# Kernel optimization log

Hardware: AMD Instinct MI355X
Metric: run time of the kernel (lower is better)

Reference implementation:

```python
import jax, jax.numpy as jnp
import numpy as np

N_ENTITIES = 100000
N_EDGES = 500000
N_RELATIONS = 200
DIM = 64
HEADS = 4
POW_ITER = 5
ALPHA = 0.1
LEAKY_SLOPE = 0.01
EPS = 1e-16


def setup_inputs() -> dict:
    key = jax.random.key(0)
    ks = jax.random.split(key, 11)
    scale = 0.1
    return {
        "entity_embed": jax.random.normal(ks[0], (N_ENTITIES, DIM), jnp.float32),
        "relation_embed": jax.random.normal(ks[1], (N_RELATIONS, DIM), jnp.float32),
        "W_h": jax.random.normal(ks[2], (DIM, HEADS * DIM), jnp.float32) * scale,
        "W_t": jax.random.normal(ks[3], (DIM, HEADS * DIM), jnp.float32) * scale,
        "W_r": jax.random.normal(ks[4], (DIM, HEADS * DIM), jnp.float32) * scale,
        "att_h": jax.random.normal(ks[5], (HEADS, DIM), jnp.float32) * scale,
        "att_t": jax.random.normal(ks[6], (HEADS, DIM), jnp.float32) * scale,
        "att_r": jax.random.normal(ks[7], (HEADS, DIM), jnp.float32) * scale,
        "W_o": jax.random.normal(ks[8], (HEADS * DIM, DIM), jnp.float32) * scale,
        "edge_index": jax.random.randint(ks[9], (2, N_EDGES), 0, N_ENTITIES, jnp.int64),
        "edge_type": jax.random.randint(ks[10], (N_EDGES,), 0, N_RELATIONS, jnp.int64),
    }


def _segment_softmax(scores, seg_ids, num_segments):
    # scores: [E, heads]; softmax over edges sharing the same seg_id, per head
    m = jax.ops.segment_max(scores, seg_ids, num_segments=num_segments)
    e = jnp.exp(scores - m[seg_ids])
    denom = jax.ops.segment_sum(e, seg_ids, num_segments=num_segments)
    return e / (denom[seg_ids] + EPS)


def reference(entity_embed, relation_embed, W_h, W_t, W_r,
              att_h, att_t, att_r, W_o, edge_index, edge_type):
    head_ids, tail_ids = edge_index[0], edge_index[1]

    # per-edge gathered embeddings, projected per head: [E, heads, dim]
    Wh = (entity_embed[head_ids] @ W_h).reshape(-1, HEADS, DIM)
    Wt = (entity_embed[tail_ids] @ W_t).reshape(-1, HEADS, DIM)
    Wr = (relation_embed[edge_type] @ W_r).reshape(-1, HEADS, DIM)

    s_h = jnp.sum(jnp.tanh(Wh) * att_h[None], axis=-1)  # [E, heads]
    s_t = jnp.sum(jnp.tanh(Wt) * att_t[None], axis=-1)
    s_r = jnp.sum(jnp.tanh(Wr) * att_r[None], axis=-1)
    scores = jax.nn.leaky_relu(s_h + s_t + s_r, negative_slope=LEAKY_SLOPE)

    att = _segment_softmax(scores, head_ids, N_ENTITIES)  # [E, heads]
    A = (1.0 - ALPHA) * att

    # PPR power iteration, vectorized over heads: Z: [N, heads, dim]
    Z0 = entity_embed[:, None, :]  # [N, 1, dim]
    Z_init = jnp.broadcast_to(Z0, (N_ENTITIES, HEADS, DIM))

    def step(Z, _):
        msgs = A[:, :, None] * Z[tail_ids]  # [E, heads, dim]
        Z_new = jax.ops.segment_sum(msgs, head_ids, num_segments=N_ENTITIES) + ALPHA * Z0
        return Z_new, None

    Z, _ = jax.lax.scan(step, Z_init, None, length=POW_ITER)

    out = Z.reshape(N_ENTITIES, HEADS * DIM) @ W_o  # [N, dim]
    return out
```

## Files before the change

### kernel.cpp

```cpp
#include <hip/hip_runtime.h>
#include <hip/hip_fp16.h>
#include <math.h>

#define N_ENT 100000
#define N_EDGE 500000
#define N_REL 200

typedef short bf16x8 __attribute__((ext_vector_type(8)));
typedef _Float16 f16x8 __attribute__((ext_vector_type(8)));
typedef float f32x4 __attribute__((ext_vector_type(4)));

__device__ __forceinline__ float fast_tanh(float x) {
    float xc = fminf(x, 15.f);
    float e = __expf(2.f * xc);
    return 1.f - 2.f * __builtin_amdgcn_rcpf(e + 1.f);
}

__device__ __forceinline__ unsigned short f2bf(float f) {
    unsigned u = __float_as_uint(f);
    unsigned r = u + 0x7FFF + ((u >> 16) & 1);
    return (unsigned short)(r >> 16);
}

__device__ __forceinline__ unsigned pack_half2(float a, float b) {
    __half2 h = __floats2half2_rn(a, b);
    return *reinterpret_cast<unsigned*>(&h);
}

#define HIST_B 1954
#define EMB_B  2048
#define WT_B   128
#define WOT_B  64
__global__ __launch_bounds__(256) void prep_kernel(
    const float* __restrict__ entity, unsigned short* __restrict__ emb_bf,
    const float* __restrict__ W0, const float* __restrict__ W1,
    unsigned short* __restrict__ wT,
    const float* __restrict__ Wo, __half* __restrict__ woT,
    const int* __restrict__ eidx, int* __restrict__ counts,
    int* __restrict__ eoff)
{
    int bid = blockIdx.x;
    if (bid < HIST_B) {
        int e = bid * 256 + threadIdx.x;
        if (e < N_EDGE) eoff[e] = atomicAdd(&counts[eidx[e]], 1);
    } else if (bid < HIST_B + EMB_B) {
        int b = bid - HIST_B;
        const int nquads = N_ENT * 64 / 4;
        for (int i = b * 256 + threadIdx.x; i < nquads; i += EMB_B * 256) {
            float4 v = ((const float4*)entity)[i];
            ushort4 o;
            o.x = f2bf(v.x); o.y = f2bf(v.y); o.z = f2bf(v.z); o.w = f2bf(v.w);
            ((ushort4*)emb_bf)[i] = o;
        }
    } else if (bid < HIST_B + EMB_B + WT_B) {
        int idx = (bid - HIST_B - EMB_B) * 256 + threadIdx.x;
        int mat = idx >> 14;
        int rem = idx & 16383;
        int col = rem >> 6;
        int k   = rem & 63;
        const float* W = (mat == 0) ? W0 : W1;
        wT[idx] = f2bf(W[k * 256 + col]);
    } else {
        int idx = (bid - HIST_B - EMB_B - WT_B) * 256 + threadIdx.x;
        int d = idx >> 8;
        int k = idx & 255;
        woT[idx] = __float2half(Wo[k * 64 + d]);
    }
}

__global__ __launch_bounds__(256) void proj_mfma_kernel(
    const unsigned short* __restrict__ emb_bf,
    const unsigned short* __restrict__ wT,
    const float* __restrict__ att0, const float* __restrict__ att1,
    float* __restrict__ p0, float* __restrict__ p1, int nrows, int nb)
{
    const int mat = (blockIdx.x >= nb) ? 1 : 0;
    const int rb  = blockIdx.x - mat * nb;
    const float* att = (mat == 0) ? att0 : att1;
    float* p         = (mat == 0) ? p0 : p1;
    const unsigned short* wbase = wT + (size_t)mat * 256 * 64;

    const int wv   = threadIdx.x >> 6;
    const int lane = threadIdx.x & 63;
    const int r4   = lane >> 4;
    const int cl   = lane & 15;
    const int rowbase = rb * 64 + wv * 16;

    int ra = min(rowbase + cl, nrows - 1);
    bf16x8 a0 = *(const bf16x8*)(emb_bf + (size_t)ra * 64 + 8 * r4);
    bf16x8 a1 = *(const bf16x8*)(emb_bf + (size_t)ra * 64 + 8 * r4 + 32);

    float pacc[4][4];
#pragma unroll
    for (int head = 0; head < 4; ++head) {
        float vsum[4] = {0.f, 0.f, 0.f, 0.f};
#pragma unroll
        for (int sub = 0; sub < 4; ++sub) {
            int col = head * 64 + sub * 16 + cl;
            const unsigned short* wp = wbase + (size_t)col * 64 + 8 * r4;
            bf16x8 b0 = *(const bf16x8*)(wp);
            bf16x8 b1 = *(const bf16x8*)(wp + 32);
            f32x4 c = {0.f, 0.f, 0.f, 0.f};
            c = __builtin_amdgcn_mfma_f32_16x16x32_bf16(a0, b0, c, 0, 0, 0);
            c = __builtin_amdgcn_mfma_f32_16x16x32_bf16(a1, b1, c, 0, 0, 0);
            float av = att[head * 64 + sub * 16 + cl];
#pragma unroll
            for (int j = 0; j < 4; ++j)
                vsum[j] = fmaf(fast_tanh(c[j]), av, vsum[j]);
        }
#pragma unroll
        for (int j = 0; j < 4; ++j) {
            float v = vsum[j];
            v += __shfl_xor(v, 1, 64);
            v += __shfl_xor(v, 2, 64);
            v += __shfl_xor(v, 4, 64);
            v += __shfl_xor(v, 8, 64);
            pacc[head][j] = v;
        }
    }
    if (cl == 0) {
#pragma unroll
        for (int j = 0; j < 4; ++j) {
            int row = rowbase + r4 * 4 + j;
            if (row < nrows) {
                *(float4*)(p + (size_t)row * 4) = make_float4(
                    pacc[0][j], pacc[1][j], pacc[2][j], pacc[3][j]);
            }
        }
    }
}

__global__ __launch_bounds__(256) void proj_gemm_kernel(
    const float* __restrict__ emb,
    const float* __restrict__ W0,
    const float* __restrict__ att0,
    float* __restrict__ p0,
    int nrows)
{
    __shared__ float e_lds[64][68];
    __shared__ float w0_lds[64][64];
    __shared__ float red[4][4][64];

    const int t    = threadIdx.x;
    const int wv   = t >> 6;
    const int lane = t & 63;
    const int er   = t & 15;
    const int d0   = (t >> 4) * 4;
    const int base = blockIdx.x * 64;

#pragma unroll
    for (int i = 0; i < 4; ++i) {
        int f = t + 256 * i;
        int row = f >> 4, c4 = f & 15;
        int gr = min(base + row, nrows - 1);
        float4 v = *(const float4*)(emb + (size_t)gr * 64 + 4 * c4);
        *(float4*)&e_lds[row][4 * c4] = v;
    }

    float p0s[4][4];

    for (int head = 0; head < 4; ++head) {
        {
            int k0 = t >> 4, c4 = t & 15;
#pragma unroll
            for (int kk = 0; kk < 4; ++kk) {
                int k = k0 + 16 * kk;
                *(float4*)&w0_lds[k][4 * c4] =
                    *(const float4*)(W0 + (size_t)k * 256 + head * 64 + 4 * c4);
            }
        }
        __syncthreads();

        float acc0[4][4] = {};
        for (int k4 = 0; k4 < 16; ++k4) {
            float4 z0 = *(const float4*)&e_lds[er +  0][4 * k4];
            float4 z1 = *(const float4*)&e_lds[er + 16][4 * k4];
            float4 z2 = *(const float4*)&e_lds[er + 32][4 * k4];
            float4 z3 = *(const float4*)&e_lds[er + 48][4 * k4];
            const float zr[4][4] = {
                {z0.x, z0.y, z0.z, z0.w},
                {z1.x, z1.y, z1.z, z1.w},
                {z2.x, z2.y, z2.z, z2.w},
                {z3.x, z3.y, z3.z, z3.w}};
#pragma unroll
            for (int jj = 0; jj < 4; ++jj) {
                float4 w0v = *(const float4*)&w0_lds[4 * k4 + jj][d0];
#pragma unroll
                for (int i = 0; i < 4; ++i) {
                    float zj = zr[i][jj];
                    acc0[i][0] = fmaf(zj, w0v.x, acc0[i][0]);
                    acc0[i][1] = fmaf(zj, w0v.y, acc0[i][1]);
                    acc0[i][2] = fmaf(zj, w0v.z, acc0[i][2]);
                    acc0[i][3] = fmaf(zj, w0v.w, acc0[i][3]);
                }
            }
        }

        float4 av0 = *(const float4*)(att0 + head * 64 + d0);
#pragma unroll
        for (int i = 0; i < 4; ++i) {
            float v = fast_tanh(acc0[i][0]) * av0.x
                    + fast_tanh(acc0[i][1]) * av0.y
                    + fast_tanh(acc0[i][2]) * av0.z
                    + fast_tanh(acc0[i][3]) * av0.w;
            v += __shfl_xor(v, 16, 64);
            v += __shfl_xor(v, 32, 64);
            p0s[head][i] = v;
        }
        __syncthreads();
    }

    if (lane < 16) {
#pragma unroll
        for (int h = 0; h < 4; ++h)
#pragma unroll
            for (int i = 0; i < 4; ++i)
                red[wv][h][lane + 16 * i] = p0s[h][i];
    }
    __syncthreads();
    if (t < 64) {
        int row = base + t;
        if (row < nrows) {
            float4 pv;
            pv.x = red[0][0][t] + red[1][0][t] + red[2][0][t] + red[3][0][t];
            pv.y = red[0][1][t] + red[1][1][t] + red[2][1][t] + red[3][1][t];
            pv.z = red[0][2][t] + red[1][2][t] + red[2][2][t] + red[3][2][t];
            pv.w = red[0][3][t] + red[1][3][t] + red[2][3][t] + red[3][3][t];
            *(float4*)(p0 + (size_t)row * 4) = pv;
        }
    }
}

__global__ __launch_bounds__(1024) void scan_kernel(
    const int* __restrict__ counts, int* __restrict__ row_start)
{
    __shared__ int wsum[16];
    __shared__ int carry_s;
    const int lane = threadIdx.x & 63;
    const int wid  = threadIdx.x >> 6;
    if (threadIdx.x == 0) carry_s = 0;
    __syncthreads();
    for (int base = 0; base < N_ENT; base += 4096) {
        int i0 = base + (int)threadIdx.x * 4;
        int4 v = make_int4(0, 0, 0, 0);
        if (i0 + 3 < N_ENT) v = *(const int4*)(counts + i0);
        else {
            if (i0 + 0 < N_ENT) v.x = counts[i0 + 0];
            if (i0 + 1 < N_ENT) v.y = counts[i0 + 1];
            if (i0 + 2 < N_ENT) v.z = counts[i0 + 2];
            if (i0 + 3 < N_ENT) v.w = counts[i0 + 3];
        }
        int s1 = v.x + v.y, s2 = s1 + v.z, tsum = s2 + v.w;
        int incl = tsum;
#pragma unroll
        for (int off = 1; off < 64; off <<= 1) {
            int t = __shfl_up(incl, off, 64);
            if (lane >= off) incl += t;
        }
        if (lane == 63) wsum[wid] = incl;
        __syncthreads();
        int wave_off = 0;
#pragma unroll
        for (int w = 0; w < 16; ++w)
            wave_off += (w < wid) ? wsum[w] : 0;
        int carry = carry_s;
        int excl = carry + wave_off + (incl - tsum);
        if (i0 + 3 < N_ENT) {
            *(int4*)(row_start + i0) = make_int4(excl, excl + v.x, excl + s1, excl + s2);
        } else {
            if (i0 + 0 < N_ENT) row_start[i0 + 0] = excl;
            if (i0 + 1 < N_ENT) row_start[i0 + 1] = excl + v.x;
            if (i0 + 2 < N_ENT) row_start[i0 + 2] = excl + s1;
            if (i0 + 3 < N_ENT) row_start[i0 + 3] = excl + s2;
        }
        __syncthreads();
        if (threadIdx.x == 1023) carry_s = carry + wave_off + incl;
    }
    __syncthreads();
    if (threadIdx.x == 0) row_start[N_ENT] = carry_s;
}

__global__ __launch_bounds__(256) void scatter_score_kernel(
    const int* __restrict__ eidx, const int* __restrict__ etype,
    const float* __restrict__ ph, const float* __restrict__ pt,
    const float* __restrict__ pr,
    const int* __restrict__ row_start, const int* __restrict__ eoff,
    int* __restrict__ csr_col, float* __restrict__ csr_a)
{
    int e = blockIdx.x * 256 + threadIdx.x;
    if (e >= N_EDGE) return;
    int hn = eidx[e];
    int tn = eidx[N_EDGE + e];
    int r  = etype[e];
    float4 a = *(const float4*)(ph + (size_t)hn * 4);
    float4 b = *(const float4*)(pt + (size_t)tn * 4);
    float4 c = *(const float4*)(pr + (size_t)r * 4);
    float s0 = a.x + b.x + c.x;
    float s1 = a.y + b.y + c.y;
    float s2 = a.z + b.z + c.z;
    float s3 = a.w + b.w + c.w;
    s0 = s0 >= 0.f ? s0 : 0.01f * s0;
    s1 = s1 >= 0.f ? s1 : 0.01f * s1;
    s2 = s2 >= 0.f ? s2 : 0.01f * s2;
    s3 = s3 >= 0.f ? s3 : 0.01f * s3;
    float4 ev = make_float4(__expf(s0), __expf(s1), __expf(s2), __expf(s3));
    int pos = row_start[hn] + eoff[e];
    csr_col[pos] = tn;
    *(float4*)(csr_a + (size_t)pos * 4) = ev;
}

template <bool IN_HALF, bool NORM>
__device__ __forceinline__ void spmm_row_pair(
    int n, int lane, float scale,
    const __half* __restrict__ Zin_h, const float* __restrict__ emb,
    const int* __restrict__ row_start, const int* __restrict__ csr_col,
    float* __restrict__ csr_a, float acc[8])
{
    const int half = lane >> 5;
    const int j    = lane & 31;
    const int hd   = j >> 3;
    const int s    = row_start[n];
    const int end  = row_start[n + 1];

    {
        const float* z0p = emb + (size_t)n * 64 + 8 * (j & 7);
        float4 z0a = *(const float4*)(z0p);
        float4 z0b = *(const float4*)(z0p + 4);
        float m = (half == 0) ? 0.1f : 0.f;
        acc[0] = m * z0a.x; acc[1] = m * z0a.y; acc[2] = m * z0a.z; acc[3] = m * z0a.w;
        acc[4] = m * z0b.x; acc[5] = m * z0b.y; acc[6] = m * z0b.z; acc[7] = m * z0b.w;
    }
    float accB[8] = {0.f, 0.f, 0.f, 0.f, 0.f, 0.f, 0.f, 0.f};

    for (int b = s; b < end; b += 16) {
        const int nb = min(16, end - b);
        int   cl = (lane < nb) ? csr_col[b + lane] : 0;
        float al = (lane < nb * 4) ? csr_a[(size_t)b * 4 + lane] : 0.f;
        if (NORM) {
            al *= scale;
            if (lane < nb * 4) csr_a[(size_t)b * 4 + lane] = al;
        }
        for (int e = 0; e < nb; e += 4) {
            int iA = half ? min(e + 1, nb - 1) : e;
            int iB = half ? min(e + 3, nb - 1) : min(e + 2, nb - 1);
            int cA = __shfl(cl, iA, 64);
            int cB = __shfl(cl, iB, 64);
            float aA = __shfl(al, iA * 4 + hd, 64);
            float aB = __shfl(al, iB * 4 + hd, 64);
            aA = (e + half < nb) ? aA : 0.f;
            aB = (e + 2 + half < nb) ? aB : 0.f;
            if (IN_HALF) {
                f16x8 zA = *(const f16x8*)(Zin_h + (size_t)cA * 256 + 8 * j);
                f16x8 zB = *(const f16x8*)(Zin_h + (size_t)cB * 256 + 8 * j);
#pragma unroll
                for (int k = 0; k < 8; ++k) {
                    acc[k]  = fmaf(aA, (float)zA[k], acc[k]);
                    accB[k] = fmaf(aB, (float)zB[k], accB[k]);
                }
            } else {
                int ec = 8 * (j & 7);
                float4 zA0 = *(const float4*)(emb + (size_t)cA * 64 + ec);
                float4 zA1 = *(const float4*)(emb + (size_t)cA * 64 + ec + 4);
                float4 zB0 = *(const float4*)(emb + (size_t)cB * 64 + ec);
                float4 zB1 = *(const float4*)(emb + (size_t)cB * 64 + ec + 4);
                acc[0] = fmaf(aA, zA0.x, acc[0]);
                acc[1] = fmaf(aA, zA0.y, acc[1]);
                acc[2] = fmaf(aA, zA0.z, acc[2]);
                acc[3] = fmaf(aA, zA0.w, acc[3]);
                acc[4] = fmaf(aA, zA1.x, acc[4]);
                acc[5] = fmaf(aA, zA1.y, acc[5]);
                acc[6] = fmaf(aA, zA1.z, acc[6]);
                acc[7] = fmaf(aA, zA1.w, acc[7]);
                accB[0] = fmaf(aB, zB0.x, accB[0]);
                accB[1] = fmaf(aB, zB0.y, accB[1]);
                accB[2] = fmaf(aB, zB0.z, accB[2]);
                accB[3] = fmaf(aB, zB0.w, accB[3]);
                accB[4] = fmaf(aB, zB1.x, accB[4]);
                accB[5] = fmaf(aB, zB1.y, accB[5]);
                accB[6] = fmaf(aB, zB1.z, accB[6]);
                accB[7] = fmaf(aB, zB1.w, accB[7]);
            }
        }
    }
#pragma unroll
    for (int k = 0; k < 8; ++k) {
        float v = acc[k] + accB[k];
        v += __shfl_xor(v, 32, 64);
        acc[k] = v;
    }
}

__device__ __forceinline__ void store_row_h(
    __half* __restrict__ dst256, int lane, const float acc[8])
{
    if (lane < 32) {
        uint4 o;
        o.x = pack_half2(acc[0], acc[1]);
        o.y = pack_half2(acc[2], acc[3]);
        o.z = pack_half2(acc[4], acc[5]);
        o.w = pack_half2(acc[6], acc[7]);
        *(uint4*)(dst256 + 8 * lane) = o;
    }
}

__global__ __launch_bounds__(256) void norm_spmm1_kernel(
    const float* __restrict__ emb,
    const int* __restrict__ row_start, const int* __restrict__ csr_col,
    float* __restrict__ csr_a, __half* __restrict__ Zout)
{
    const int wave = threadIdx.x >> 6;
    const int lane = threadIdx.x & 63;
    const int n = blockIdx.x * 4 + wave;
    const int s   = row_start[n];
    const int end = row_start[n + 1];
    const int nf  = (end - s) * 4;

    float sum = 0.f;
    for (int f = lane; f < nf; f += 64)
        sum += csr_a[(size_t)s * 4 + f];
#pragma unroll
    for (int off = 4; off < 64; off <<= 1)
        sum += __shfl_xor(sum, off, 64);
    float scale = 0.9f * __builtin_amdgcn_rcpf(sum + 1e-16f);

    float acc[8];
    spmm_row_pair<false, true>(n, lane, scale, nullptr, emb,
                               row_start, csr_col, csr_a, acc);
    store_row_h(Zout + (size_t)n * 256, lane, acc);
}

__global__ __launch_bounds__(256) void spmm_kernel(
    const __half* __restrict__ Zin, const float* __restrict__ emb,
    const int* __restrict__ row_start, const int* __restrict__ csr_col,
    float* __restrict__ csr_a, __half* __restrict__ Zout)
{
    const int wave = threadIdx.x >> 6;
    const int lane = threadIdx.x & 63;
    const int n = blockIdx.x * 4 + wave;
    float acc[8];
    spmm_row_pair<true, false>(n, lane, 1.f, Zin, emb,
                               row_start, csr_col, csr_a, acc);
    store_row_h(Zout + (size_t)n * 256, lane, acc);
}

__global__ __launch_bounds__(256) void spmm_out_fused_kernel(
    const __half* __restrict__ Zin, const float* __restrict__ emb,
    const int* __restrict__ row_start, const int* __restrict__ csr_col,
    float* __restrict__ csr_a,
    const __half* __restrict__ woT,
    float* __restrict__ out)
{
    __shared__ _Float16 zl[16][264];
    const int wv   = threadIdx.x >> 6;
    const int lane = threadIdx.x & 63;
    const int base = blockIdx.x * 16;

#pragma unroll
    for (int rr = 0; rr < 4; ++rr) {
        int n = base + wv * 4 + rr;
        float acc[8];
        spmm_row_pair<true, false>(n, lane, 1.f, Zin, emb,
                                   row_start, csr_col, csr_a, acc);
        if (lane < 32) {
            uint4 o;
            o.x = pack_half2(acc[0], acc[1]);
            o.y = pack_half2(acc[2], acc[3]);
            o.z = pack_half2(acc[4], acc[5]);
            o.w = pack_half2(acc[6], acc[7]);
            *(uint4*)&zl[wv * 4 + rr][8 * lane] = o;
        }
    }
    __syncthreads();

    const int cl = lane & 15;
    const int r4 = lane >> 4;
    f16x8 a[8];
#pragma unroll
    for (int ks = 0; ks < 8; ++ks)
        a[ks] = *(const f16x8*)&zl[cl][ks * 32 + 8 * r4];

    const _Float16* wcol = (const _Float16*)woT + (size_t)(wv * 16 + cl) * 256 + 8 * r4;
    f32x4 c = {0.f, 0.f, 0.f, 0.f};
#pragma unroll
    for (int ks = 0; ks < 8; ++ks) {
        f16x8 b = *(const f16x8*)(wcol + ks * 32);
        c = __builtin_amdgcn_mfma_f32_16x16x32_f16(a[ks], b, c, 0, 0, 0);
    }
#pragma unroll
    for (int j = 0; j < 4; ++j) {
        int row = base + r4 * 4 + j;
        out[(size_t)row * 64 + wv * 16 + cl] = c[j];
    }
}

extern "C" void kernel_launch(void* const* d_in, const int* in_sizes, int n_in,
                              void* d_out, int out_size, void* d_ws, size_t ws_size,
                              hipStream_t stream)
{
    const float* entity = (const float*)d_in[0];
    const float* rel    = (const float*)d_in[1];
    const float* W_h    = (const float*)d_in[2];
    const float* W_t    = (const float*)d_in[3];
    const float* W_r    = (const float*)d_in[4];
    const float* att_h  = (const float*)d_in[5];
    const float* att_t  = (const float*)d_in[6];
    const float* att_r  = (const float*)d_in[7];
    const float* W_o    = (const float*)d_in[8];
    const int*   eidx   = (const int*)d_in[9];
    const int*   etype  = (const int*)d_in[10];
    float* out = (float*)d_out;

    char* ws = (char*)d_ws;
    size_t off = 0;
    auto alloc = [&](size_t bytes) -> void* {
        void* p = ws + off;
        off += (bytes + 255) & ~(size_t)255;
        return p;
    };
    float* p_h      = (float*)alloc((size_t)N_ENT * 4 * 4);
    float* p_t      = (float*)alloc((size_t)N_ENT * 4 * 4);
    float* p_r      = (float*)alloc((size_t)N_REL * 4 * 4);
    int*   counts   = (int*)alloc((size_t)N_ENT * 4);
    int*   row_start= (int*)alloc(((size_t)N_ENT + 1) * 4);
    int*   eoff     = (int*)alloc((size_t)N_EDGE * 4);
    int*   csr_col  = (int*)alloc((size_t)N_EDGE * 4);
    float* csr_a    = (float*)alloc((size_t)N_EDGE * 4 * 4);
    __half* Zh_a    = (__half*)alloc((size_t)N_ENT * 256 * 2);
    __half* Zh_b    = (__half*)alloc((size_t)N_ENT * 256 * 2);
    unsigned short* emb_bf = (unsigned short*)alloc((size_t)N_ENT * 64 * 2);
    unsigned short* wT     = (unsigned short*)alloc((size_t)2 * 256 * 64 * 2);
    __half* woT     = (__half*)alloc((size_t)64 * 256 * 2);

    hipMemsetAsync(counts, 0, (size_t)N_ENT * 4, stream);

    prep_kernel<<<HIST_B + EMB_B + WT_B + WOT_B, 256, 0, stream>>>(
        entity, emb_bf, W_h, W_t, wT, W_o, woT, eidx, counts, eoff);

    const int nb = (N_ENT + 63) / 64;
    proj_mfma_kernel<<<2 * nb, 256, 0, stream>>>(
        emb_bf, wT, att_h, att_t, p_h, p_t, N_ENT, nb);
    proj_gemm_kernel<<<(N_REL + 63) / 64, 256, 0, stream>>>(
        rel, W_r, att_r, p_r, N_REL);

    scan_kernel<<<1, 1024, 0, stream>>>(counts, row_start);
    scatter_score_kernel<<<(N_EDGE + 255) / 256, 256, 0, stream>>>(
        eidx, etype, p_h, p_t, p_r, row_start, eoff, csr_col, csr_a);

    norm_spmm1_kernel<<<N_ENT / 4, 256, 0, stream>>>(
        entity, row_start, csr_col, csr_a, Zh_b);
    spmm_kernel<<<N_ENT / 4, 256, 0, stream>>>(Zh_b, entity, row_start, csr_col, csr_a, Zh_a);
    spmm_kernel<<<N_ENT / 4, 256, 0, stream>>>(Zh_a, entity, row_start, csr_col, csr_a, Zh_b);
    spmm_kernel<<<N_ENT / 4, 256, 0, stream>>>(Zh_b, entity, row_start, csr_col, csr_a, Zh_a);
    spmm_out_fused_kernel<<<N_ENT / 16, 256, 0, stream>>>(
        Zh_a, entity, row_start, csr_col, csr_a, woT, out);
}
```

Baseline: 405.0 us.

## Split SpMM power iterations per head with row-per-8-lanes mapping and fp16 embeddings

Restructures the PPR sparse propagation. A separate normalize kernel rescales the attention weights. Each power iteration now runs as four per-head launches, so the gathered working set for a launch is one 64-wide head slice, which should fit better in L2/infinity cache. Each wave handles 8 rows with 8 lanes per row and walks edges serially. The entity embeddings are also precomputed in fp16, which shrinks the first-iteration gathers and the Z0 reads. This adds 12 extra launches and gives up the per-wave edge-parallel batching, so long rows become serial. The Z0 term loses some precision from the fp16 embeddings.

```diff
diff --git a/kernel.cpp b/kernel.cpp
--- a/kernel.cpp
+++ b/kernel.cpp
@@ -33,6 +33,7 @@
 #define WOT_B  64
 __global__ __launch_bounds__(256) void prep_kernel(
     const float* __restrict__ entity, unsigned short* __restrict__ emb_bf,
+    __half* __restrict__ emb_h,
     const float* __restrict__ W0, const float* __restrict__ W1,
     unsigned short* __restrict__ wT,
     const float* __restrict__ Wo, __half* __restrict__ woT,
@@ -51,6 +52,10 @@
             ushort4 o;
             o.x = f2bf(v.x); o.y = f2bf(v.y); o.z = f2bf(v.z); o.w = f2bf(v.w);
             ((ushort4*)emb_bf)[i] = o;
+            uint2 oh;
+            oh.x = pack_half2(v.x, v.y);
+            oh.y = pack_half2(v.z, v.w);
+            ((uint2*)emb_h)[i] = oh;
         }
     } else if (bid < HIST_B + EMB_B + WT_B) {
         int idx = (bid - HIST_B - EMB_B) * 256 + threadIdx.x;
@@ -309,166 +314,106 @@
     *(float4*)(csr_a + (size_t)pos * 4) = ev;
 }
 
-template <bool IN_HALF, bool NORM>
-__device__ __forceinline__ void spmm_row_pair(
-    int n, int lane, float scale,
-    const __half* __restrict__ Zin_h, const float* __restrict__ emb,
+__global__ __launch_bounds__(256) void normalize_kernel(
+    const int* __restrict__ row_start, float* __restrict__ csr_a)
+{
+    const int wid  = threadIdx.x >> 6;
+    const int lane = threadIdx.x & 63;
+    const int n = blockIdx.x * 4 + wid;
+    if (n >= N_ENT) return;
+    const int s   = row_start[n];
+    const int end = row_start[n + 1];
+    const int nf  = (end - s) * 4;
+
+    float sum = 0.f;
+    for (int f = lane; f < nf; f += 64)
+        sum += csr_a[(size_t)s * 4 + f];
+#pragma unroll
+    for (int off = 4; off < 64; off <<= 1)
+        sum += __shfl_xor(sum, off, 64);
+    float scale = 0.9f * __builtin_amdgcn_rcpf(sum + 1e-16f);
+    for (int f = lane; f < nf; f += 64)
+        csr_a[(size_t)s * 4 + f] *= scale;
+}
+
+template <bool FIRST>
+__global__ __launch_bounds__(256) void spmm_head_kernel(
+    const __half* __restrict__ Zin,
+    const __half* __restrict__ emb_h,
     const int* __restrict__ row_start, const int* __restrict__ csr_col,
-    float* __restrict__ csr_a, float acc[8])
-{
-    const int half = lane >> 5;
-    const int j    = lane & 31;
-    const int hd   = j >> 3;
-    const int s    = row_start[n];
-    const int end  = row_start[n + 1];
-
+    const float* __restrict__ csr_a, __half* __restrict__ Zout, int phase)
+{
+    const int wave = threadIdx.x >> 6;
+    const int lane = threadIdx.x & 63;
+    const int r = lane >> 3;
+    const int c = lane & 7;
+    const int n = (blockIdx.x * 4 + wave) * 8 + r;
+    if (n >= N_ENT) return;
+
+    const _Float16* zin = (const _Float16*)Zin;
+    float acc[8];
     {
-        const float* z0p = emb + (size_t)n * 64 + 8 * (j & 7);
-        float4 z0a = *(const float4*)(z0p);
-        float4 z0b = *(const float4*)(z0p + 4);
-        float m = (half == 0) ? 0.1f : 0.f;
-        acc[0] = m * z0a.x; acc[1] = m * z0a.y; acc[2] = m * z0a.z; acc[3] = m * z0a.w;
-        acc[4] = m * z0b.x; acc[5] = m * z0b.y; acc[6] = m * z0b.z; acc[7] = m * z0b.w;
-    }
-    float accB[8] = {0.f, 0.f, 0.f, 0.f, 0.f, 0.f, 0.f, 0.f};
-
-    for (int b = s; b < end; b += 16) {
-        const int nb = min(16, end - b);
-        int   cl = (lane < nb) ? csr_col[b + lane] : 0;
-        float al = (lane < nb * 4) ? csr_a[(size_t)b * 4 + lane] : 0.f;
-        if (NORM) {
-            al *= scale;
-            if (lane < nb * 4) csr_a[(size_t)b * 4 + lane] = al;
-        }
-        for (int e = 0; e < nb; e += 4) {
-            int iA = half ? min(e + 1, nb - 1) : e;
-            int iB = half ? min(e + 3, nb - 1) : min(e + 2, nb - 1);
-            int cA = __shfl(cl, iA, 64);
-            int cB = __shfl(cl, iB, 64);
-            float aA = __shfl(al, iA * 4 + hd, 64);
-            float aB = __shfl(al, iB * 4 + hd, 64);
-            aA = (e + half < nb) ? aA : 0.f;
-            aB = (e + 2 + half < nb) ? aB : 0.f;
-            if (IN_HALF) {
-                f16x8 zA = *(const f16x8*)(Zin_h + (size_t)cA * 256 + 8 * j);
-                f16x8 zB = *(const f16x8*)(Zin_h + (size_t)cB * 256 + 8 * j);
-#pragma unroll
-                for (int k = 0; k < 8; ++k) {
-                    acc[k]  = fmaf(aA, (float)zA[k], acc[k]);
-                    accB[k] = fmaf(aB, (float)zB[k], accB[k]);
-                }
-            } else {
-                int ec = 8 * (j & 7);
-                float4 zA0 = *(const float4*)(emb + (size_t)cA * 64 + ec);
-                float4 zA1 = *(const float4*)(emb + (size_t)cA * 64 + ec + 4);
-                float4 zB0 = *(const float4*)(emb + (size_t)cB * 64 + ec);
-                float4 zB1 = *(const float4*)(emb + (size_t)cB * 64 + ec + 4);
-                acc[0] = fmaf(aA, zA0.x, acc[0]);
-                acc[1] = fmaf(aA, zA0.y, acc[1]);
-                acc[2] = fmaf(aA, zA0.z, acc[2]);
-                acc[3] = fmaf(aA, zA0.w, acc[3]);
-                acc[4] = fmaf(aA, zA1.x, acc[4]);
-                acc[5] = fmaf(aA, zA1.y, acc[5]);
-                acc[6] = fmaf(aA, zA1.z, acc[6]);
-                acc[7] = fmaf(aA, zA1.w, acc[7]);
-                accB[0] = fmaf(aB, zB0.x, accB[0]);
-                accB[1] = fmaf(aB, zB0.y, accB[1]);
-                accB[2] = fmaf(aB, zB0.z, accB[2]);
-                accB[3] = fmaf(aB, zB0.w, accB[3]);
-                accB[4] = fmaf(aB, zB1.x, accB[4]);
-                accB[5] = fmaf(aB, zB1.y, accB[5]);
-                accB[6] = fmaf(aB, zB1.z, accB[6]);
-                accB[7] = fmaf(aB, zB1.w, accB[7]);
-            }
-        }
-    }
-#pragma unroll
-    for (int k = 0; k < 8; ++k) {
-        float v = acc[k] + accB[k];
-        v += __shfl_xor(v, 32, 64);
-        acc[k] = v;
-    }
-}
-
-__device__ __forceinline__ void store_row_h(
-    __half* __restrict__ dst256, int lane, const float acc[8])
-{
-    if (lane < 32) {
+        f16x8 z0 = *(const f16x8*)((const _Float16*)emb_h + (size_t)n * 64 + 8 * c);
+#pragma unroll
+        for (int k = 0; k < 8; ++k) acc[k] = 0.1f * (float)z0[k];
+    }
+    const int s = row_start[n], end = row_start[n + 1];
+    for (int e = s; e < end; ++e) {
+        float a  = csr_a[(size_t)e * 4 + phase];
+        int col  = csr_col[e];
+        const _Float16* zp = FIRST
+            ? zin + (size_t)col * 64 + 8 * c
+            : zin + (size_t)col * 256 + phase * 64 + 8 * c;
+        f16x8 z = *(const f16x8*)zp;
+#pragma unroll
+        for (int k = 0; k < 8; ++k) acc[k] = fmaf(a, (float)z[k], acc[k]);
+    }
+    uint4 o;
+    o.x = pack_half2(acc[0], acc[1]);
+    o.y = pack_half2(acc[2], acc[3]);
+    o.z = pack_half2(acc[4], acc[5]);
+    o.w = pack_half2(acc[6], acc[7]);
+    *(uint4*)((_Float16*)Zout + (size_t)n * 256 + phase * 64 + 8 * c) = o;
+}
+
+__global__ __launch_bounds__(256) void spmm_out_fused_kernel(
+    const __half* __restrict__ Zin, const __half* __restrict__ emb_h,
+    const int* __restrict__ row_start, const int* __restrict__ csr_col,
+    const float* __restrict__ csr_a,
+    const __half* __restrict__ woT,
+    float* __restrict__ out)
+{
+    __shared__ _Float16 zl[16][264];
+    const int wv   = threadIdx.x >> 6;
+    const int lane = threadIdx.x & 63;
+    const int r = lane >> 3;
+    const int c = lane & 7;
+    const int base = blockIdx.x * 16;
+    const _Float16* zin = (const _Float16*)Zin;
+
+#pragma unroll
+    for (int half16 = 0; half16 < 2; ++half16) {
+        const int n = base + half16 * 8 + r;
+        float acc[8];
+        {
+            f16x8 z0 = *(const f16x8*)((const _Float16*)emb_h + (size_t)n * 64 + 8 * c);
+#pragma unroll
+            for (int k = 0; k < 8; ++k) acc[k] = 0.1f * (float)z0[k];
+        }
+        const int s = row_start[n], end = row_start[n + 1];
+        for (int e = s; e < end; ++e) {
+            float a = csr_a[(size_t)e * 4 + wv];
+            int col = csr_col[e];
+            f16x8 z = *(const f16x8*)(zin + (size_t)col * 256 + wv * 64 + 8 * c);
+#pragma unroll
+            for (int k = 0; k < 8; ++k) acc[k] = fmaf(a, (float)z[k], acc[k]);
+        }
         uint4 o;
         o.x = pack_half2(acc[0], acc[1]);
         o.y = pack_half2(acc[2], acc[3]);
         o.z = pack_half2(acc[4], acc[5]);
         o.w = pack_half2(acc[6], acc[7]);
-        *(uint4*)(dst256 + 8 * lane) = o;
-    }
-}
-
-__global__ __launch_bounds__(256) void norm_spmm1_kernel(
-    const float* __restrict__ emb,
-    const int* __restrict__ row_start, const int* __restrict__ csr_col,
-    float* __restrict__ csr_a, __half* __restrict__ Zout)
-{
-    const int wave = threadIdx.x >> 6;
-    const int lane = threadIdx.x & 63;
-    const int n = blockIdx.x * 4 + wave;
-    const int s   = row_start[n];
-    const int end = row_start[n + 1];
-    const int nf  = (end - s) * 4;
-
-    float sum = 0.f;
-    for (int f = lane; f < nf; f += 64)
-        sum += csr_a[(size_t)s * 4 + f];
-#pragma unroll
-    for (int off = 4; off < 64; off <<= 1)
-        sum += __shfl_xor(sum, off, 64);
-    float scale = 0.9f * __builtin_amdgcn_rcpf(sum + 1e-16f);
-
-    float acc[8];
-    spmm_row_pair<false, true>(n, lane, scale, nullptr, emb,
-                               row_start, csr_col, csr_a, acc);
-    store_row_h(Zout + (size_t)n * 256, lane, acc);
-}
-
-__global__ __launch_bounds__(256) void spmm_kernel(
-    const __half* __restrict__ Zin, const float* __restrict__ emb,
-    const int* __restrict__ row_start, const int* __restrict__ csr_col,
-    float* __restrict__ csr_a, __half* __restrict__ Zout)
-{
-    const int wave = threadIdx.x >> 6;
-    const int lane = threadIdx.x & 63;
-    const int n = blockIdx.x * 4 + wave;
-    float acc[8];
-    spmm_row_pair<true, false>(n, lane, 1.f, Zin, emb,
-                               row_start, csr_col, csr_a, acc);
-    store_row_h(Zout + (size_t)n * 256, lane, acc);
-}
-
-__global__ __launch_bounds__(256) void spmm_out_fused_kernel(
-    const __half* __restrict__ Zin, const float* __restrict__ emb,
-    const int* __restrict__ row_start, const int* __restrict__ csr_col,
-    float* __restrict__ csr_a,
-    const __half* __restrict__ woT,
-    float* __restrict__ out)
-{
-    __shared__ _Float16 zl[16][264];
-    const int wv   = threadIdx.x >> 6;
-    const int lane = threadIdx.x & 63;
-    const int base = blockIdx.x * 16;
-
-#pragma unroll
-    for (int rr = 0; rr < 4; ++rr) {
-        int n = base + wv * 4 + rr;
-        float acc[8];
-        spmm_row_pair<true, false>(n, lane, 1.f, Zin, emb,
-                                   row_start, csr_col, csr_a, acc);
-        if (lane < 32) {
-            uint4 o;
-            o.x = pack_half2(acc[0], acc[1]);
-            o.y = pack_half2(acc[2], acc[3]);
-            o.z = pack_half2(acc[4], acc[5]);
-            o.w = pack_half2(acc[6], acc[7]);
-            *(uint4*)&zl[wv * 4 + rr][8 * lane] = o;
-        }
+        *(uint4*)&zl[half16 * 8 + r][wv * 64 + 8 * c] = o;
     }
     __syncthreads();
 
@@ -480,16 +425,16 @@
         a[ks] = *(const f16x8*)&zl[cl][ks * 32 + 8 * r4];
 
     const _Float16* wcol = (const _Float16*)woT + (size_t)(wv * 16 + cl) * 256 + 8 * r4;
-    f32x4 c = {0.f, 0.f, 0.f, 0.f};
+    f32x4 cc = {0.f, 0.f, 0.f, 0.f};
 #pragma unroll
     for (int ks = 0; ks < 8; ++ks) {
         f16x8 b = *(const f16x8*)(wcol + ks * 32);
-        c = __builtin_amdgcn_mfma_f32_16x16x32_f16(a[ks], b, c, 0, 0, 0);
+        cc = __builtin_amdgcn_mfma_f32_16x16x32_f16(a[ks], b, cc, 0, 0, 0);
     }
 #pragma unroll
     for (int j = 0; j < 4; ++j) {
         int row = base + r4 * 4 + j;
-        out[(size_t)row * 64 + wv * 16 + cl] = c[j];
+        out[(size_t)row * 64 + wv * 16 + cl] = cc[j];
     }
 }
 
@@ -528,13 +473,14 @@
     __half* Zh_a    = (__half*)alloc((size_t)N_ENT * 256 * 2);
     __half* Zh_b    = (__half*)alloc((size_t)N_ENT * 256 * 2);
     unsigned short* emb_bf = (unsigned short*)alloc((size_t)N_ENT * 64 * 2);
+    __half* emb_h   = (__half*)alloc((size_t)N_ENT * 64 * 2);
     unsigned short* wT     = (unsigned short*)alloc((size_t)2 * 256 * 64 * 2);
     __half* woT     = (__half*)alloc((size_t)64 * 256 * 2);
 
     hipMemsetAsync(counts, 0, (size_t)N_ENT * 4, stream);
 
     prep_kernel<<<HIST_B + EMB_B + WT_B + WOT_B, 256, 0, stream>>>(
-        entity, emb_bf, W_h, W_t, wT, W_o, woT, eidx, counts, eoff);
+        entity, emb_bf, emb_h, W_h, W_t, wT, W_o, woT, eidx, counts, eoff);
 
     const int nb = (N_ENT + 63) / 64;
     proj_mfma_kernel<<<2 * nb, 256, 0, stream>>>(
@@ -545,12 +491,21 @@
     scan_kernel<<<1, 1024, 0, stream>>>(counts, row_start);
     scatter_score_kernel<<<(N_EDGE + 255) / 256, 256, 0, stream>>>(
         eidx, etype, p_h, p_t, p_r, row_start, eoff, csr_col, csr_a);
-
-    norm_spmm1_kernel<<<N_ENT / 4, 256, 0, stream>>>(
-        entity, row_start, csr_col, csr_a, Zh_b);
-    spmm_kernel<<<N_ENT / 4, 256, 0, stream>>>(Zh_b, entity, row_start, csr_col, csr_a, Zh_a);
-    spmm_kernel<<<N_ENT / 4, 256, 0, stream>>>(Zh_a, entity, row_start, csr_col, csr_a, Zh_b);
-    spmm_kernel<<<N_ENT / 4, 256, 0, stream>>>(Zh_b, entity, row_start, csr_col, csr_a, Zh_a);
+    normalize_kernel<<<(N_ENT + 3) / 4, 256, 0, stream>>>(row_start, csr_a);
+
+    const int sg = (N_ENT + 31) / 32;
+    for (int ph = 0; ph < 4; ++ph)
+        spmm_head_kernel<true><<<sg, 256, 0, stream>>>(
+            emb_h, emb_h, row_start, csr_col, csr_a, Zh_b, ph);
+    for (int ph = 0; ph < 4; ++ph)
+        spmm_head_kernel<false><<<sg, 256, 0, stream>>>(
+            Zh_b, emb_h, row_start, csr_col, csr_a, Zh_a, ph);
+    for (int ph = 0; ph < 4; ++ph)
+        spmm_head_kernel<false><<<sg, 256, 0, stream>>>(
+            Zh_a, emb_h, row_start, csr_col, csr_a, Zh_b, ph);
+    for (int ph = 0; ph < 4; ++ph)
+        spmm_head_kernel<false><<<sg, 256, 0, stream>>>(
+            Zh_b, emb_h, row_start, csr_col, csr_a, Zh_a, ph);
     spmm_out_fused_kernel<<<N_ENT / 16, 256, 0, stream>>>(
-        Zh_a, entity, row_start, csr_col, csr_a, woT, out);
-}
+        Zh_a, emb_h, row_start, csr_col, csr_a, woT, out);
+}
```

New measurement: 574.1 us. 41.7% more time.
